# Kernel optimization log

Hardware: AMD Instinct MI355X
Metric: run time of the kernel (lower is better)

Reference implementation:

```python
import jax, jax.numpy as jnp
import numpy as np

D_IN = 2048
H1 = D_IN // 4      # 512
H2 = D_IN // 16     # 128
N_EXP = 8
N_CLS = 10
BATCH = 16384


def setup_inputs() -> dict:
    key = jax.random.key(0)
    ks = jax.random.split(key, 16)
    s = lambda k, shape, fan_in: jax.random.normal(k, shape, jnp.float32) / np.sqrt(fan_in)
    return {
        "fs": jax.random.normal(ks[0], (BATCH, D_IN // 2), jnp.float32),
        "fp": jax.random.normal(ks[1], (BATCH, D_IN // 2), jnp.float32),
        # gate MLP params (output = num_source, softmax)
        "gW1": s(ks[2], (D_IN, H1), D_IN), "gb1": jnp.zeros((H1,), jnp.float32),
        "gW2": s(ks[3], (H1, H2), H1),     "gb2": jnp.zeros((H2,), jnp.float32),
        "gW3": s(ks[4], (H2, N_EXP), H2), "gb3": jnp.zeros((N_EXP,), jnp.float32),
        # stacked expert MLP params (output = num classes, log_softmax)
        "eW1": s(ks[5], (N_EXP, D_IN, H1), D_IN), "eb1": jnp.zeros((N_EXP, H1), jnp.float32),
        "eW2": s(ks[6], (N_EXP, H1, H2), H1),     "eb2": jnp.zeros((N_EXP, H2), jnp.float32),
        "eW3": s(ks[7], (N_EXP, H2, N_CLS), H2),  "eb3": jnp.zeros((N_EXP, N_CLS), jnp.float32),
    }


def reference(fs, fp, gW1, gb1, gW2, gb2, gW3, gb3, eW1, eb1, eW2, eb2, eW3, eb3):
    features = jnp.concatenate([fs, fp], axis=-1)            # [B, D_IN]

    # Gate MLP on detached features (detach is a no-op for fwd), softmax output
    g = jax.nn.relu(features @ gW1 + gb1)
    g = jax.nn.relu(g @ gW2 + gb2)
    gate_outs = jax.nn.softmax(g @ gW3 + gb3, axis=-1)       # [B, E]

    # All experts as batched GEMMs over stacked weights, log_softmax output
    h = jax.nn.relu(jnp.einsum('bd,edh->beh', features, eW1) + eb1[None])   # [B, E, H1]
    h = jax.nn.relu(jnp.einsum('beh,ehk->bek', h, eW2) + eb2[None])         # [B, E, H2]
    logits = jnp.einsum('bek,eko->beo', h, eW3) + eb3[None]                 # [B, E, C]
    expert_outs = jax.nn.log_softmax(logits, axis=-1)                       # [B, E, C]

    # Gate-weighted sum over experts
    output = jnp.einsum('be,bec->bc', gate_outs, expert_outs)               # [B, C]
    return output, gate_outs
```

## Files before the change

### kernel.cpp

```cpp
#include <hip/hip_runtime.h>
#include <hip/hip_bf16.h>

#define B_SZ   16384
#define DIN    2048
#define H1_SZ  512
#define H2_SZ  128
#define N_EXP  8
#define N_CLS  10
#define N1     4608
#define N2     1152

typedef __attribute__((ext_vector_type(8))) __bf16 bf16x8;
typedef __attribute__((ext_vector_type(4))) float  floatx4;
typedef __attribute__((ext_vector_type(4))) short  short4v;
typedef __attribute__((ext_vector_type(8))) short  short8v;

__device__ __forceinline__ float bf2f(short s) {
  unsigned int u = ((unsigned int)(unsigned short)s) << 16;
  float f; __builtin_memcpy(&f, &u, 4); return f;
}

__global__ void convert_features_kernel(const float* __restrict__ fs,
                                        const float* __restrict__ fp,
                                        __hip_bfloat16* __restrict__ X) {
  const int nf4 = B_SZ * (DIN / 4);
  const float4* fs4 = (const float4*)fs;
  const float4* fp4 = (const float4*)fp;
  for (int i = blockIdx.x * blockDim.x + threadIdx.x; i < nf4;
       i += gridDim.x * blockDim.x) {
    int c = i & 511;
    int row = i >> 9;
    float4 v = (c < 256) ? fs4[(size_t)row * 256 + c]
                         : fp4[(size_t)row * 256 + (c - 256)];
    union { short4v v4; __hip_bfloat16 h[4]; } u;
    u.h[0] = __float2bfloat16(v.x);
    u.h[1] = __float2bfloat16(v.y);
    u.h[2] = __float2bfloat16(v.z);
    u.h[3] = __float2bfloat16(v.w);
    *(short4v*)(X + (size_t)i * 4) = u.v4;
  }
}

__global__ void transpose_convert_kernel(const float* __restrict__ expert_src,
                                         const float* __restrict__ gate_src,
                                         int K, int H, int E,
                                         __hip_bfloat16* __restrict__ out) {
  __shared__ float t[32][33];
  int k0 = blockIdx.x * 32;
  int n0 = blockIdx.y * 32;
  int e = n0 / H;
  const float* src; int h0;
  if (e < E) { src = expert_src + (size_t)e * K * H; h0 = n0 - e * H; }
  else       { src = gate_src;                       h0 = n0 - E * H; }
  int tx = threadIdx.x, ty = threadIdx.y;
  #pragma unroll
  for (int j = 0; j < 4; ++j) {
    int r = ty + j * 8;
    t[r][tx] = src[(size_t)(k0 + r) * H + h0 + tx];
  }
  __syncthreads();
  #pragma unroll
  for (int j = 0; j < 4; ++j) {
    int r = ty + j * 8;
    out[(size_t)(n0 + r) * K + k0 + tx] = __float2bfloat16(t[tx][r]);
  }
}

__device__ __forceinline__ void gemm_core(
    const __hip_bfloat16* __restrict__ A,  int lda,
    const __hip_bfloat16* __restrict__ BT, int K,
    const float* __restrict__ bias,
    __hip_bfloat16* __restrict__ O, int ldo) {
  __shared__ __align__(16) __hip_bfloat16 As[128 * 64];
  __shared__ __align__(16) __hip_bfloat16 Bs[128 * 64];

  const int tid  = threadIdx.x;
  const int lane = tid & 63;
  const int wave = tid >> 6;
  const int wm   = (wave >> 1) * 64;
  const int wn   = (wave & 1) * 64;
  const int lrow  = lane & 15;
  const int lquad = lane >> 4;

  floatx4 acc[4][4] = {};

  for (int k0 = 0; k0 < K; k0 += 64) {
    #pragma unroll
    for (int j = 0; j < 4; ++j) {
      int chunk = j * 256 + tid;
      int mi = chunk >> 3;
      int cs = chunk & 7;
      int cl = cs ^ (mi & 7);
      __builtin_amdgcn_global_load_lds(
          (const __attribute__((address_space(1))) unsigned int*)(A + (size_t)mi * lda + k0 + cl * 8),
          (__attribute__((address_space(3))) unsigned int*)(As + chunk * 8),
          16, 0, 0);
      __builtin_amdgcn_global_load_lds(
          (const __attribute__((address_space(1))) unsigned int*)(BT + (size_t)mi * K + k0 + cl * 8),
          (__attribute__((address_space(3))) unsigned int*)(Bs + chunk * 8),
          16, 0, 0);
    }
    __syncthreads();
    #pragma unroll
    for (int ks = 0; ks < 2; ++ks) {
      bf16x8 a[4], b[4];
      #pragma unroll
      for (int t = 0; t < 4; ++t) {
        int ar = wm + t * 16 + lrow;
        int br = wn + t * 16 + lrow;
        int ca = (ks * 4 + lquad) ^ (ar & 7);
        int cb = (ks * 4 + lquad) ^ (br & 7);
        a[t] = *(const bf16x8*)(As + ar * 64 + ca * 8);
        b[t] = *(const bf16x8*)(Bs + br * 64 + cb * 8);
      }
      #pragma unroll
      for (int mt = 0; mt < 4; ++mt)
        #pragma unroll
        for (int nt = 0; nt < 4; ++nt)
          acc[mt][nt] = __builtin_amdgcn_mfma_f32_16x16x32_bf16(
              a[mt], b[nt], acc[mt][nt], 0, 0, 0);
    }
    __syncthreads();
  }

  #pragma unroll
  for (int nt = 0; nt < 4; ++nt) {
    int col = wn + nt * 16 + lrow;
    float bv = bias[col];
    #pragma unroll
    for (int mt = 0; mt < 4; ++mt) {
      #pragma unroll
      for (int r = 0; r < 4; ++r) {
        int row = wm + mt * 16 + lquad * 4 + r;
        float v = acc[mt][nt][r] + bv;
        v = v > 0.f ? v : 0.f;
        O[(size_t)row * ldo + col] = __float2bfloat16(v);
      }
    }
  }
}

__global__ __launch_bounds__(256, 2) void gemm1_kernel(
    const __hip_bfloat16* __restrict__ X, const __hip_bfloat16* __restrict__ W1T,
    const float* __restrict__ eb1, const float* __restrict__ gb1,
    __hip_bfloat16* __restrict__ H1) {
  int m0 = blockIdx.y * 128;
  int n0 = blockIdx.x * 128;
  const float* bias = (n0 < N_EXP * H1_SZ) ? (eb1 + n0) : (gb1 + (n0 - N_EXP * H1_SZ));
  gemm_core(X + (size_t)m0 * DIN, DIN,
            W1T + (size_t)n0 * DIN, DIN,
            bias,
            H1 + (size_t)m0 * N1 + n0, N1);
}

__global__ __launch_bounds__(256, 2) void gemm2_kernel(
    const __hip_bfloat16* __restrict__ H1, const __hip_bfloat16* __restrict__ W2T,
    const float* __restrict__ eb2, const float* __restrict__ gb2,
    __hip_bfloat16* __restrict__ H2) {
  int m0 = blockIdx.y * 128;
  int z  = blockIdx.z;
  const float* bias = (z < N_EXP) ? (eb2 + z * H2_SZ) : gb2;
  gemm_core(H1 + (size_t)m0 * N1 + z * H1_SZ, N1,
            W2T + (size_t)z * H2_SZ * H1_SZ, H1_SZ,
            bias,
            H2 + (size_t)m0 * N2 + z * H2_SZ, N2);
}

__global__ __launch_bounds__(256) void layer3_kernel(
    const __hip_bfloat16* __restrict__ H2,
    const float* __restrict__ gW3, const float* __restrict__ gb3,
    const float* __restrict__ eW3, const float* __restrict__ eb3,
    float* __restrict__ out, float* __restrict__ gate_out) {
  int tid  = threadIdx.x;
  int j    = tid & 7;
  int rloc = tid >> 3;
  long row = (long)blockIdx.x * 32 + rloc;
  const __hip_bfloat16* hrow = H2 + row * N2;

  float accg = 0.f;
  float acc[N_CLS];
  #pragma unroll
  for (int c = 0; c < N_CLS; ++c) acc[c] = 0.f;

  #pragma unroll 4
  for (int k8 = 0; k8 < 16; ++k8) {
    short8v hg8 = *(const short8v*)(hrow + N_EXP * H2_SZ + k8 * 8);
    short8v he8 = *(const short8v*)(hrow + j * H2_SZ + k8 * 8);
    #pragma unroll
    for (int t = 0; t < 8; ++t) {
      int k = k8 * 8 + t;
      float hg = bf2f(hg8[t]);
      float he = bf2f(he8[t]);
      accg += hg * gW3[k * N_EXP + j];
      const float* w = eW3 + (size_t)(j * H2_SZ + k) * N_CLS;
      #pragma unroll
      for (int c = 0; c < N_CLS; ++c) acc[c] += he * w[c];
    }
  }

  float gj = accg + gb3[j];
  float mx = gj;
  mx = fmaxf(mx, __shfl_xor(mx, 1));
  mx = fmaxf(mx, __shfl_xor(mx, 2));
  mx = fmaxf(mx, __shfl_xor(mx, 4));
  float ex = __expf(gj - mx);
  float s = ex;
  s += __shfl_xor(s, 1);
  s += __shfl_xor(s, 2);
  s += __shfl_xor(s, 4);
  float gp = ex / s;

  float lg[N_CLS];
  float lm = -1e30f;
  #pragma unroll
  for (int c = 0; c < N_CLS; ++c) {
    lg[c] = acc[c] + eb3[j * N_CLS + c];
    lm = fmaxf(lm, lg[c]);
  }
  float es = 0.f;
  #pragma unroll
  for (int c = 0; c < N_CLS; ++c) es += __expf(lg[c] - lm);
  float lse = lm + __logf(es);

  float o[N_CLS];
  #pragma unroll
  for (int c = 0; c < N_CLS; ++c) o[c] = gp * (lg[c] - lse);
  #pragma unroll
  for (int c = 0; c < N_CLS; ++c) {
    o[c] += __shfl_xor(o[c], 1);
    o[c] += __shfl_xor(o[c], 2);
    o[c] += __shfl_xor(o[c], 4);
  }

  gate_out[row * N_EXP + j] = gp;
  if (j == 0) {
    #pragma unroll
    for (int c = 0; c < N_CLS; ++c) out[row * N_CLS + c] = o[c];
  }
}

extern "C" void kernel_launch(void* const* d_in, const int* in_sizes, int n_in,
                              void* d_out, int out_size, void* d_ws, size_t ws_size,
                              hipStream_t stream) {
  const float* fs  = (const float*)d_in[0];
  const float* fp  = (const float*)d_in[1];
  const float* gW1 = (const float*)d_in[2];
  const float* gb1 = (const float*)d_in[3];
  const float* gW2 = (const float*)d_in[4];
  const float* gb2 = (const float*)d_in[5];
  const float* gW3 = (const float*)d_in[6];
  const float* gb3 = (const float*)d_in[7];
  const float* eW1 = (const float*)d_in[8];
  const float* eb1 = (const float*)d_in[9];
  const float* eW2 = (const float*)d_in[10];
  const float* eb2 = (const float*)d_in[11];
  const float* eW3 = (const float*)d_in[12];
  const float* eb3 = (const float*)d_in[13];
  float* out = (float*)d_out;

  char* ws = (char*)d_ws;
  __hip_bfloat16* X   = (__hip_bfloat16*)ws;
  __hip_bfloat16* H2  = X;
  __hip_bfloat16* W1T = (__hip_bfloat16*)(ws + 67108864);
  __hip_bfloat16* W2T = (__hip_bfloat16*)(ws + 85983232);
  __hip_bfloat16* H1  = (__hip_bfloat16*)(ws + 87162880);

  convert_features_kernel<<<2048, 256, 0, stream>>>(fs, fp, X);
  transpose_convert_kernel<<<dim3(DIN / 32, N1 / 32), dim3(32, 8), 0, stream>>>(
      eW1, gW1, DIN, H1_SZ, N_EXP, W1T);
  transpose_convert_kernel<<<dim3(H1_SZ / 32, N2 / 32), dim3(32, 8), 0, stream>>>(
      eW2, gW2, H1_SZ, H2_SZ, N_EXP, W2T);
  gemm1_kernel<<<dim3(N1 / 128, B_SZ / 128), 256, 0, stream>>>(X, W1T, eb1, gb1, H1);
  gemm2_kernel<<<dim3(1, B_SZ / 128, N_EXP + 1), 256, 0, stream>>>(H1, W2T, eb2, gb2, H2);
  layer3_kernel<<<B_SZ / 32, 256, 0, stream>>>(H2, gW3, gb3, eW3, eb3,
                                               out, out + (size_t)B_SZ * N_CLS);
}
```

Before: 602.3 us.

## Merge prep kernels, swap GEMM1 grid order, raise GEMM occupancy bound

```diff
diff --git a/kernel.cpp b/kernel.cpp
--- a/kernel.cpp
+++ b/kernel.cpp
@@ -20,49 +20,60 @@
   float f; __builtin_memcpy(&f, &u, 4); return f;
 }
 
-__global__ void convert_features_kernel(const float* __restrict__ fs,
-                                        const float* __restrict__ fp,
-                                        __hip_bfloat16* __restrict__ X) {
-  const int nf4 = B_SZ * (DIN / 4);
-  const float4* fs4 = (const float4*)fs;
-  const float4* fp4 = (const float4*)fp;
-  for (int i = blockIdx.x * blockDim.x + threadIdx.x; i < nf4;
-       i += gridDim.x * blockDim.x) {
-    int c = i & 511;
-    int row = i >> 9;
-    float4 v = (c < 256) ? fs4[(size_t)row * 256 + c]
-                         : fp4[(size_t)row * 256 + (c - 256)];
-    union { short4v v4; __hip_bfloat16 h[4]; } u;
-    u.h[0] = __float2bfloat16(v.x);
-    u.h[1] = __float2bfloat16(v.y);
-    u.h[2] = __float2bfloat16(v.z);
-    u.h[3] = __float2bfloat16(v.w);
-    *(short4v*)(X + (size_t)i * 4) = u.v4;
-  }
-}
-
-__global__ void transpose_convert_kernel(const float* __restrict__ expert_src,
-                                         const float* __restrict__ gate_src,
-                                         int K, int H, int E,
-                                         __hip_bfloat16* __restrict__ out) {
-  __shared__ float t[32][33];
-  int k0 = blockIdx.x * 32;
-  int n0 = blockIdx.y * 32;
-  int e = n0 / H;
-  const float* src; int h0;
-  if (e < E) { src = expert_src + (size_t)e * K * H; h0 = n0 - e * H; }
-  else       { src = gate_src;                       h0 = n0 - E * H; }
-  int tx = threadIdx.x, ty = threadIdx.y;
-  #pragma unroll
-  for (int j = 0; j < 4; ++j) {
-    int r = ty + j * 8;
-    t[r][tx] = src[(size_t)(k0 + r) * H + h0 + tx];
-  }
-  __syncthreads();
-  #pragma unroll
-  for (int j = 0; j < 4; ++j) {
-    int r = ty + j * 8;
-    out[(size_t)(n0 + r) * K + k0 + tx] = __float2bfloat16(t[tx][r]);
+__global__ __launch_bounds__(256) void prep_kernel(
+    const float* __restrict__ fs, const float* __restrict__ fp,
+    const float* __restrict__ eW1, const float* __restrict__ gW1,
+    const float* __restrict__ eW2, const float* __restrict__ gW2,
+    __hip_bfloat16* __restrict__ X,
+    __hip_bfloat16* __restrict__ W1T,
+    __hip_bfloat16* __restrict__ W2T) {
+  __shared__ float tbuf[32][33];
+  const int b   = blockIdx.x;
+  const int tid = threadIdx.x;
+
+  if (b < 2048) {
+    const int nf4 = B_SZ * (DIN / 4);
+    const float4* fs4 = (const float4*)fs;
+    const float4* fp4 = (const float4*)fp;
+    for (int i = b * 256 + tid; i < nf4; i += 2048 * 256) {
+      int c = i & 511;
+      int row = i >> 9;
+      float4 v = (c < 256) ? fs4[(size_t)row * 256 + c]
+                           : fp4[(size_t)row * 256 + (c - 256)];
+      union { short4v v4; __hip_bfloat16 h[4]; } u;
+      u.h[0] = __float2bfloat16(v.x);
+      u.h[1] = __float2bfloat16(v.y);
+      u.h[2] = __float2bfloat16(v.z);
+      u.h[3] = __float2bfloat16(v.w);
+      *(short4v*)(X + (size_t)i * 4) = u.v4;
+    }
+  } else {
+    const float* esrc; const float* gsrc; __hip_bfloat16* out;
+    int K, H, bx, by;
+    if (b < 2048 + 9216) {
+      int t = b - 2048;  bx = t & 63; by = t >> 6;
+      esrc = eW1; gsrc = gW1; out = W1T; K = DIN; H = H1_SZ;
+    } else {
+      int t = b - 11264; bx = t & 15; by = t >> 4;
+      esrc = eW2; gsrc = gW2; out = W2T; K = H1_SZ; H = H2_SZ;
+    }
+    int k0 = bx * 32, n0 = by * 32;
+    int e = n0 / H;
+    const float* src; int h0;
+    if (e < N_EXP) { src = esrc + (size_t)e * K * H; h0 = n0 - e * H; }
+    else           { src = gsrc;                     h0 = n0 - N_EXP * H; }
+    int tx = tid & 31, ty = tid >> 5;
+    #pragma unroll
+    for (int j = 0; j < 4; ++j) {
+      int r = ty + j * 8;
+      tbuf[r][tx] = src[(size_t)(k0 + r) * H + h0 + tx];
+    }
+    __syncthreads();
+    #pragma unroll
+    for (int j = 0; j < 4; ++j) {
+      int r = ty + j * 8;
+      out[(size_t)(n0 + r) * K + k0 + tx] = __float2bfloat16(tbuf[tx][r]);
+    }
   }
 }
 
@@ -140,12 +151,12 @@
   }
 }
 
-__global__ __launch_bounds__(256, 2) void gemm1_kernel(
+__global__ __launch_bounds__(256, 4) void gemm1_kernel(
     const __hip_bfloat16* __restrict__ X, const __hip_bfloat16* __restrict__ W1T,
     const float* __restrict__ eb1, const float* __restrict__ gb1,
     __hip_bfloat16* __restrict__ H1) {
-  int m0 = blockIdx.y * 128;
-  int n0 = blockIdx.x * 128;
+  int m0 = blockIdx.x * 128;
+  int n0 = blockIdx.y * 128;
   const float* bias = (n0 < N_EXP * H1_SZ) ? (eb1 + n0) : (gb1 + (n0 - N_EXP * H1_SZ));
   gemm_core(X + (size_t)m0 * DIN, DIN,
             W1T + (size_t)n0 * DIN, DIN,
@@ -153,7 +164,7 @@
             H1 + (size_t)m0 * N1 + n0, N1);
 }
 
-__global__ __launch_bounds__(256, 2) void gemm2_kernel(
+__global__ __launch_bounds__(256, 4) void gemm2_kernel(
     const __hip_bfloat16* __restrict__ H1, const __hip_bfloat16* __restrict__ W2T,
     const float* __restrict__ eb2, const float* __restrict__ gb2,
     __hip_bfloat16* __restrict__ H2) {
@@ -265,12 +276,8 @@
   __hip_bfloat16* W2T = (__hip_bfloat16*)(ws + 85983232);
   __hip_bfloat16* H1  = (__hip_bfloat16*)(ws + 87162880);
 
-  convert_features_kernel<<<2048, 256, 0, stream>>>(fs, fp, X);
-  transpose_convert_kernel<<<dim3(DIN / 32, N1 / 32), dim3(32, 8), 0, stream>>>(
-      eW1, gW1, DIN, H1_SZ, N_EXP, W1T);
-  transpose_convert_kernel<<<dim3(H1_SZ / 32, N2 / 32), dim3(32, 8), 0, stream>>>(
-      eW2, gW2, H1_SZ, H2_SZ, N_EXP, W2T);
-  gemm1_kernel<<<dim3(N1 / 128, B_SZ / 128), 256, 0, stream>>>(X, W1T, eb1, gb1, H1);
+  prep_kernel<<<11840, 256, 0, stream>>>(fs, fp, eW1, gW1, eW2, gW2, X, W1T, W2T);
+  gemm1_kernel<<<dim3(B_SZ / 128, N1 / 128), 256, 0, stream>>>(X, W1T, eb1, gb1, H1);
   gemm2_kernel<<<dim3(1, B_SZ / 128, N_EXP + 1), 256, 0, stream>>>(H1, W2T, eb2, gb2, H2);
   layer3_kernel<<<B_SZ / 32, 256, 0, stream>>>(H2, gW3, gb3, eW3, eb3,
                                                out, out + (size_t)B_SZ * N_CLS);
```

Result: no change. 612.2 us (+1.6%).
